# Optimization experiments

Measured on AMD Instinct MI355X. Metric: run time of the kernel, lower is better.

## Reference

```python
import jax, jax.numpy as jnp
import numpy as np

EPS = 1e-10

def _mlp(x, W1, b1, W2, b2):
    # Linear -> ReLU -> Linear (matches _MultiLayerPercep)
    return jnp.maximum(x @ W1 + b1, 0.0) @ W2 + b2

def setup_inputs() -> dict:
    key = jax.random.key(0)
    ks = jax.random.split(key, 24)
    B, P, Q, P2, D = 512, 100, 40, 40, 64
    Nu, Ni, Nr = 100000, 100000, 6

    def lin(k, fi, fo):
        kw, kb = jax.random.split(k)
        s = 1.0 / np.sqrt(fi)
        return (jax.random.uniform(kw, (fi, fo), jnp.float32, -s, s),
                jax.random.uniform(kb, (fo,), jnp.float32, -s, s))

    uids = jax.random.randint(ks[0], (B,), 0, Nu)
    u_item_pad = jnp.stack([jax.random.randint(ks[1], (B, P), 0, Ni),
                            jax.random.randint(ks[2], (B, P), 0, Nr)], axis=-1)
    u_user_pad = jax.random.randint(ks[3], (B, Q), 0, Nu)
    u_user_item_pad = jnp.stack([jax.random.randint(ks[4], (B, Q, P2), 0, Ni),
                                 jax.random.randint(ks[5], (B, Q, P2), 0, Nr)], axis=-1)

    user_table = jax.random.normal(ks[6], (Nu, D), jnp.float32) * 0.1
    item_table = jax.random.normal(ks[7], (Ni, D), jnp.float32) * 0.1
    rate_table = jax.random.normal(ks[8], (Nr, D), jnp.float32) * 0.1

    gv_W1, gv_b1 = lin(ks[9], 2 * D, D)
    gv_W2, gv_b2 = lin(ks[10], D, D)
    atti_W1, atti_b1 = lin(ks[11], 2 * D, D)
    atti_W2, atti_b2 = lin(ks[12], D, 1)
    agg_W, agg_b = lin(ks[13], D, D)
    attu_W1, attu_b1 = lin(ks[14], 2 * D, D)
    attu_W2, attu_b2 = lin(ks[15], D, 1)
    aggn_W, aggn_b = lin(ks[16], D, D)
    cm_W1, cm_b1 = lin(ks[17], 2 * D, D)
    cm_W2, cm_b2 = lin(ks[18], D, D)
    cm_W3, cm_b3 = lin(ks[19], D, D)

    return dict(uids=uids, u_item_pad=u_item_pad, u_user_pad=u_user_pad,
                u_user_item_pad=u_user_item_pad,
                user_table=user_table, item_table=item_table, rate_table=rate_table,
                gv_W1=gv_W1, gv_b1=gv_b1, gv_W2=gv_W2, gv_b2=gv_b2,
                atti_W1=atti_W1, atti_b1=atti_b1, atti_W2=atti_W2, atti_b2=atti_b2,
                agg_W=agg_W, agg_b=agg_b,
                attu_W1=attu_W1, attu_b1=attu_b1, attu_W2=attu_W2, attu_b2=attu_b2,
                aggn_W=aggn_W, aggn_b=aggn_b,
                cm_W1=cm_W1, cm_b1=cm_b1, cm_W2=cm_W2, cm_b2=cm_b2, cm_W3=cm_W3, cm_b3=cm_b3)

def reference(uids, u_item_pad, u_user_pad, u_user_item_pad,
              user_table, item_table, rate_table,
              gv_W1, gv_b1, gv_W2, gv_b2,
              atti_W1, atti_b1, atti_W2, atti_b2,
              agg_W, agg_b,
              attu_W1, attu_b1, attu_W2, attu_b2,
              aggn_W, aggn_b,
              cm_W1, cm_b1, cm_W2, cm_b2, cm_W3, cm_b3):
    f32 = jnp.float32

    # ---- item aggregation branch ----
    q_a = item_table[u_item_pad[:, :, 0]]                      # [B,P,D]
    mask_u = (u_item_pad[:, :, 0] > 0).astype(f32)             # [B,P]
    er = rate_table[u_item_pad[:, :, 1]]                       # [B,P,D]
    x_ia = _mlp(jnp.concatenate([q_a, er], -1), gv_W1, gv_b1, gv_W2, gv_b2)
    p_i = mask_u[..., None] * user_table[uids][:, None, :]     # [B,P,D]
    alpha = _mlp(jnp.concatenate([x_ia, p_i], -1), atti_W1, atti_b1, atti_W2, atti_b2)[..., 0]
    alpha = jnp.exp(alpha) * mask_u
    alpha = alpha / (jnp.sum(alpha, axis=1, keepdims=True) + EPS)
    h_iI = jnp.maximum(jnp.sum(alpha[..., None] * x_ia, axis=1) @ agg_W + agg_b, 0.0)  # [B,D]

    # ---- social branch: per-neighbor item aggregation ----
    q_a_s = item_table[u_user_item_pad[:, :, :, 0]]            # [B,Q,P2,D]
    mask_s = (u_user_item_pad[:, :, :, 0] > 0).astype(f32)     # [B,Q,P2]
    er_s = rate_table[u_user_item_pad[:, :, :, 1]]
    x_ia_s = _mlp(jnp.concatenate([q_a_s, er_s], -1), gv_W1, gv_b1, gv_W2, gv_b2)
    nbr_emb = user_table[u_user_pad]                           # [B,Q,D]
    p_i_s = mask_s[..., None] * nbr_emb[:, :, None, :]
    alpha_s = _mlp(jnp.concatenate([x_ia_s, p_i_s], -1), atti_W1, atti_b1, atti_W2, atti_b2)[..., 0]
    alpha_s = jnp.exp(alpha_s) * mask_s
    alpha_s = alpha_s / (jnp.sum(alpha_s, axis=2, keepdims=True) + EPS)
    h_oI = jnp.maximum(jnp.sum(alpha_s[..., None] * x_ia_s, axis=2) @ agg_W + agg_b, 0.0)  # [B,Q,D]

    # ---- social attention over neighbors ----
    beta = _mlp(jnp.concatenate([h_oI, nbr_emb], -1), attu_W1, attu_b1, attu_W2, attu_b2)[..., 0]
    mask_su = (u_user_pad > 0).astype(f32)
    beta = jnp.exp(beta) * mask_su
    beta = beta / (jnp.sum(beta, axis=1, keepdims=True) + EPS)
    h_iS = jnp.maximum(jnp.sum(beta[..., None] * h_oI, axis=1) @ aggn_W + aggn_b, 0.0)  # [B,D]

    # ---- combine ----
    h = jnp.maximum(jnp.concatenate([h_iI, h_iS], -1) @ cm_W1 + cm_b1, 0.0)
    h = jnp.maximum(h @ cm_W2 + cm_b2, 0.0)
    h = jnp.maximum(h @ cm_W3 + cm_b3, 0.0)
    return h
```

## Files before the change

kernel.cpp:

```cpp
#include <hip/hip_runtime.h>
#include <math.h>

#define EPSV 1e-10f

typedef _Float16 f16x8 __attribute__((ext_vector_type(8)));
typedef _Float16 f16x4 __attribute__((ext_vector_type(4)));
typedef float f32x4 __attribute__((ext_vector_type(4)));

#define OFF_W1T  0
#define OFF_W2T  16384
#define OFF_M2T  24576
#define OFF_X    32768
#define OFF_V    49152
#define SMEM_SZ  54272

__device__ __forceinline__ f16x8 cvt_f16x8(const float4 a, const float4 b) {
  f16x8 h;
  h[0] = (_Float16)a.x; h[1] = (_Float16)a.y; h[2] = (_Float16)a.z; h[3] = (_Float16)a.w;
  h[4] = (_Float16)b.x; h[5] = (_Float16)b.y; h[6] = (_Float16)b.z; h[7] = (_Float16)b.w;
  return h;
}

__global__ __launch_bounds__(256, 2) void agg_kernel(
    const int nSblk,
    const int* __restrict__ idsS, const int* __restrict__ uidS,
    const int* __restrict__ idsI, const int* __restrict__ uidI,
    const float* __restrict__ user_table, const float* __restrict__ item_table,
    const float* __restrict__ rate_table,
    const float* __restrict__ gv_W1, const float* __restrict__ gv_b1,
    const float* __restrict__ gv_W2, const float* __restrict__ gv_b2,
    const float* __restrict__ atti_W1, const float* __restrict__ atti_b1,
    const float* __restrict__ atti_W2, const float* __restrict__ atti_b2,
    const float* __restrict__ agg_W, const float* __restrict__ agg_b,
    float* __restrict__ outS, float* __restrict__ outI) {
  __shared__ __align__(16) char smem[SMEM_SZ];
  const int tid = threadIdx.x;
  const int wave = tid >> 6, lane = tid & 63;
  const int quad = lane >> 4, mrow = lane & 15;

  const bool isS = (int)blockIdx.x < nSblk;
  const int NG = isS ? 16 : 4;
  const int P = isS ? 40 : 100;
  const int nGrp = isS ? 4 : 1;
  const int tpg = isS ? 3 : 8;
  const int* __restrict__ ids = isS ? idsS : idsI;
  const int* __restrict__ uidp = isS ? uidS : uidI;
  float* __restrict__ out = isS ? outS : outI;
  const int gbase = isS ? (int)blockIdx.x * 16 : ((int)blockIdx.x - nSblk) * 4;

  float* sV = (float*)(smem + OFF_V);
  char* smX = smem + OFF_X;
  char* smXw = smX + wave * 4096;
  float* csW = (float*)smXw;

  {
    float* uS = (float*)smX;
    float* AU = (float*)(smem + OFF_W1T);
    for (int t = tid; t < NG * 64; t += 256) {
      const int g = t >> 6, f = t & 63;
      uS[t] = user_table[(size_t)uidp[gbase + g] * 64 + f];
    }
    for (int o = tid; o < 1024; o += 256) {
      const int k = o >> 4, fb = o & 15;
      const float4 v = ((const float4*)(atti_W1 + (64 + k) * 64))[fb];
      const float* vp = (const float*)&v;
#pragma unroll
      for (int c = 0; c < 4; ++c) {
        const int j = fb * 4 + c;
        AU[j * 64 + (((k >> 2) ^ (j & 15)) << 2) + (k & 3)] = vp[c];
      }
    }
  }
  __syncthreads();
  {
    const float4* u4 = (const float4*)smX;
    const float4* a4 = (const float4*)(smem + OFF_W1T);
    for (int t = tid; t < NG * 64; t += 256) {
      const int g = t >> 6, j = t & 63;
      float s = 0.f;
#pragma unroll 4
      for (int kb = 0; kb < 16; ++kb) {
        const float4 uu = u4[g * 16 + kb];
        const float4 aa = a4[j * 16 + (kb ^ (j & 15))];
        s += uu.x * aa.x + uu.y * aa.y + uu.z * aa.z + uu.w * aa.w;
      }
      sV[t] = s;
    }
  }
  __syncthreads();
  {
    for (int o = tid; o < 2048; o += 256) {
      const int k = o >> 4, fb = o & 15;
      const float4 v = ((const float4*)(gv_W1 + k * 64))[fb];
      const float* vp = (const float*)&v;
#pragma unroll
      for (int c = 0; c < 4; ++c) {
        const int n = fb * 4 + c;
        *(_Float16*)(smem + OFF_W1T + n * 256 + ((((k >> 3) ^ (n & 7))) << 4) +
                     ((k & 7) << 1)) = (_Float16)vp[c];
      }
    }
    for (int o = tid; o < 1024; o += 256) {
      const int h = o >> 4, fb = o & 15;
      const float4 v = ((const float4*)(gv_W2 + h * 64))[fb];
      const float* vp = (const float*)&v;
#pragma unroll
      for (int c = 0; c < 4; ++c) {
        const int n = fb * 4 + c;
        *(_Float16*)(smem + OFF_W2T + n * 128 + ((((h >> 3) ^ (n & 7))) << 4) +
                     ((h & 7) << 1)) = (_Float16)vp[c];
      }
    }
    float* sCstP = (float*)smX;
    const int n = tid & 63, jh = tid >> 6;
    float p = 0.f;
#pragma unroll 4
    for (int jj = 0; jj < 16; ++jj) {
      const int j = jh * 16 + jj;
      p = fmaf(gv_b2[j], atti_W1[j * 64 + n], p);
    }
    sCstP[jh * 64 + n] = p;
  }
  float b1r[16], b2v[4], aw2v[4];
#pragma unroll
  for (int nt = 0; nt < 4; ++nt) {
#pragma unroll
    for (int rg = 0; rg < 4; ++rg) b1r[nt * 4 + rg] = gv_b1[nt * 16 + quad * 4 + rg];
    b2v[nt] = gv_b2[nt * 16 + mrow];
    aw2v[nt] = atti_W2[nt * 16 + mrow];
  }
  const float ab2 = atti_b2[0];

  float4 pf[8];
  float pm;
  auto do_prefetch = [&](int gi2, int tt2) {
    const int g2 = gbase + wave + 4 * gi2;
    const int it = tt2 * 16 + mrow;
    int iid = 0, rid = 0;
    float m = 0.f;
    if (it < P) {
      const int2 pr = ((const int2*)ids)[(size_t)g2 * P + it];
      iid = pr.x; rid = pr.y;
      m = pr.x > 0 ? 1.f : 0.f;
    }
    pm = m;
    const float* ib = item_table + (size_t)iid * 64 + quad * 8;
    const float* rb = rate_table + (size_t)rid * 64 + quad * 8;
    pf[0] = ((const float4*)ib)[0];        pf[1] = ((const float4*)ib)[1];
    pf[2] = ((const float4*)(ib + 32))[0]; pf[3] = ((const float4*)(ib + 32))[1];
    pf[4] = ((const float4*)rb)[0];        pf[5] = ((const float4*)rb)[1];
    pf[6] = ((const float4*)(rb + 32))[0]; pf[7] = ((const float4*)(rb + 32))[1];
  };
  do_prefetch(0, 0);
  __syncthreads();
  float cstv[4];
  {
    f16x8 aM[2];
#pragma unroll
    for (int ks = 0; ks < 2; ++ks) {
      f16x8 t;
#pragma unroll
      for (int j = 0; j < 8; ++j)
        t[j] = (_Float16)atti_W1[(ks * 32 + quad * 8 + j) * 64 + (wave * 16 + mrow)];
      aM[ks] = t;
    }
#pragma unroll
    for (int ht = 0; ht < 4; ++ht) {
      f32x4 c = {0.f, 0.f, 0.f, 0.f};
#pragma unroll
      for (int ks = 0; ks < 2; ++ks) {
        const float* s = gv_W2 + (ht * 16 + mrow) * 64 + ks * 32 + quad * 8;
        f16x8 b;
#pragma unroll
        for (int j = 0; j < 8; ++j) b[j] = (_Float16)s[j];
        c = __builtin_amdgcn_mfma_f32_16x16x32_f16(aM[ks], b, c, 0, 0, 0);
      }
      const int h = ht * 16 + mrow;
#pragma unroll
      for (int rg = 0; rg < 4; ++rg) {
        const int n3 = wave * 16 + quad * 4 + rg;
        *(_Float16*)(smem + OFF_M2T + n3 * 128 + ((((h >> 3) ^ (n3 & 7))) << 4) +
                     ((h & 7) << 1)) = (_Float16)c[rg];
      }
    }
    const float* sCstP = (const float*)smX;
#pragma unroll
    for (int nt = 0; nt < 4; ++nt) {
      const int n = nt * 16 + mrow;
      cstv[nt] = atti_b1[n] + sCstP[n] + sCstP[64 + n] + sCstP[128 + n] +
                 sCstP[192 + n];
    }
  }
  __syncthreads();

  f16x8 aW[4][4], bMr[4][2];
#pragma unroll
  for (int nt = 0; nt < 4; ++nt) {
#pragma unroll
    for (int ks = 0; ks < 4; ++ks)
      aW[nt][ks] = *(const f16x8*)(smem + OFF_W1T + (nt * 16 + mrow) * 256 +
                                   (((ks * 4 + quad) ^ (mrow & 7)) << 4));
#pragma unroll
    for (int ks = 0; ks < 2; ++ks)
      bMr[nt][ks] = *(const f16x8*)(smem + OFF_M2T + (nt * 16 + mrow) * 128 +
                                    (((ks * 4 + quad) ^ (mrow & 7)) << 4));
  }

  for (int gi = 0; gi < nGrp; ++gi) {
    const int g = wave + 4 * gi;
    float vv[4];
#pragma unroll
    for (int nt = 0; nt < 4; ++nt) vv[nt] = sV[g * 64 + nt * 16 + mrow];
    float pnum[4] = {0.f, 0.f, 0.f, 0.f};
    float pden = 0.f;
    for (int tt = 0; tt < tpg; ++tt) {
      f16x8 bIn[4];
      bIn[0] = cvt_f16x8(pf[0], pf[1]);
      bIn[1] = cvt_f16x8(pf[2], pf[3]);
      bIn[2] = cvt_f16x8(pf[4], pf[5]);
      bIn[3] = cvt_f16x8(pf[6], pf[7]);
      const float mcur = pm;
      {
        int ngi = gi, ntt = tt + 1;
        if (ntt == tpg) { ntt = 0; ngi = gi + 1; }
        if (ngi < nGrp) do_prefetch(ngi, ntt);
      }
#pragma unroll
      for (int nt = 0; nt < 4; ++nt) {
        f32x4 c = {0.f, 0.f, 0.f, 0.f};
#pragma unroll
        for (int ks = 0; ks < 4; ++ks)
          c = __builtin_amdgcn_mfma_f32_16x16x32_f16(aW[nt][ks], bIn[ks], c, 0, 0, 0);
        f16x4 hv;
#pragma unroll
        for (int rg = 0; rg < 4; ++rg)
          hv[rg] = (_Float16)fmaxf(c[rg] + b1r[nt * 4 + rg], 0.f);
        *(f16x4*)(smXw + mrow * 256 +
                  (((nt * 2 + (quad >> 1)) ^ (mrow & 7)) << 4) +
                  ((quad & 1) << 3)) = hv;
      }
      f16x8 a2[2];
#pragma unroll
      for (int ks = 0; ks < 2; ++ks)
        a2[ks] = *(const f16x8*)(smXw + mrow * 256 +
                                 (((ks * 4 + quad) ^ (mrow & 7)) << 4));
      float mk[4];
#pragma unroll
      for (int rg = 0; rg < 4; ++rg) mk[rg] = __shfl(mcur, quad * 4 + rg);
      f32x4 x2a[4];
      float tl[4] = {0.f, 0.f, 0.f, 0.f};
#pragma unroll
      for (int nt = 0; nt < 4; ++nt) {
        f32x4 c = {0.f, 0.f, 0.f, 0.f}, d = {0.f, 0.f, 0.f, 0.f};
#pragma unroll
        for (int ks = 0; ks < 2; ++ks) {
          const f16x8 bW = *(const f16x8*)(smem + OFF_W2T + (nt * 16 + mrow) * 128 +
                                           (((ks * 4 + quad) ^ (mrow & 7)) << 4));
          c = __builtin_amdgcn_mfma_f32_16x16x32_f16(a2[ks], bW, c, 0, 0, 0);
        }
#pragma unroll
        for (int ks = 0; ks < 2; ++ks)
          d = __builtin_amdgcn_mfma_f32_16x16x32_f16(a2[ks], bMr[nt][ks], d, 0, 0, 0);
#pragma unroll
        for (int rg = 0; rg < 4; ++rg) x2a[nt][rg] = c[rg] + b2v[nt];
#pragma unroll
        for (int rg = 0; rg < 4; ++rg) {
          const float hh = fmaxf(d[rg] + cstv[nt] + mk[rg] * vv[nt], 0.f);
          tl[rg] = fmaf(hh, aw2v[nt], tl[rg]);
        }
      }
      float e[4];
#pragma unroll
      for (int rg = 0; rg < 4; ++rg) {
        float t = tl[rg];
        t += __shfl_xor(t, 1); t += __shfl_xor(t, 2);
        t += __shfl_xor(t, 4); t += __shfl_xor(t, 8);
        e[rg] = __expf(t + ab2) * mk[rg];
        pden += e[rg];
      }
#pragma unroll
      for (int nt = 0; nt < 4; ++nt) {
        pnum[nt] = fmaf(e[0], x2a[nt][0], pnum[nt]);
        pnum[nt] = fmaf(e[1], x2a[nt][1], pnum[nt]);
        pnum[nt] = fmaf(e[2], x2a[nt][2], pnum[nt]);
        pnum[nt] = fmaf(e[3], x2a[nt][3], pnum[nt]);
      }
    }
    float dsum = pden;
    dsum += __shfl_xor(dsum, 16); dsum += __shfl_xor(dsum, 32);
    const float rd = 1.f / (dsum + EPSV);
#pragma unroll
    for (int nt = 0; nt < 4; ++nt) {
      float s = pnum[nt];
      s += __shfl_xor(s, 16); s += __shfl_xor(s, 32);
      if (quad == 0) csW[nt * 16 + mrow] = s * rd;
    }
    float acc = agg_b[lane];
#pragma unroll 8
    for (int k = 0; k < 64; ++k) acc = fmaf(csW[k], agg_W[k * 64 + lane], acc);
    out[(size_t)(gbase + g) * 64 + lane] = fmaxf(acc, 0.f);
  }
}

#define S2_W1T 0
#define S2_X   17408
#define S2_E   26112
#define S2_MSK 26240
#define S2_HB  26368
#define S2_SZ  27904

__global__ __launch_bounds__(128, 2) void stage2_kernel(
    const int* __restrict__ u_user_pad, const float* __restrict__ user_table,
    const float* __restrict__ hoI, const float* __restrict__ hiI,
    const float* __restrict__ attu_W1, const float* __restrict__ attu_b1,
    const float* __restrict__ attu_W2, const float* __restrict__ attu_b2,
    const float* __restrict__ aggn_W, const float* __restrict__ aggn_b,
    const float* __restrict__ cm_W1, const float* __restrict__ cm_b1,
    const float* __restrict__ cm_W2, const float* __restrict__ cm_b2,
    const float* __restrict__ cm_W3, const float* __restrict__ cm_b3,
    float* __restrict__ out) {
  __shared__ __align__(16) char smem[S2_SZ];
  const int tid = threadIdx.x;
  const int wave = tid >> 6, lane = tid & 63;
  const int quad = lane >> 4, mrow = lane & 15;
  const int b = (int)blockIdx.x * 2 + wave;

  char* sW1 = smem + S2_W1T;
  char* sXw = smem + S2_X + wave * 4352;
  float* sE = (float*)(smem + S2_E) + wave * 16;
  float* sM = (float*)(smem + S2_MSK) + wave * 16;
  float* sB = (float*)(smem + S2_HB) + wave * 192;

  for (int o = tid; o < 2048; o += 128) {
    const int k = o >> 4, fb = o & 15;
    const float4 v = ((const float4*)(attu_W1 + k * 64))[fb];
    const float* vp = (const float*)&v;
#pragma unroll
    for (int c = 0; c < 4; ++c) {
      const int n = fb * 4 + c;
      *(_Float16*)(sW1 + n * 272 + ((k >> 3) << 4) + ((k & 7) << 1)) = (_Float16)vp[c];
    }
  }
  float b1v[4], w2v[4];
#pragma unroll
  for (int nt = 0; nt < 4; ++nt) {
    b1v[nt] = attu_b1[nt * 16 + mrow];
    w2v[nt] = attu_W2[nt * 16 + mrow];
  }
  const float b2s = attu_b2[0];

  float4 pa[4], pb[4];
  float msk[4];
  auto pf = [&](int tt) {
#pragma unroll
    for (int k = 0; k < 4; ++k) {
      const int u = lane + (k << 6);
      const int r = u >> 4, bb = u & 15;
      const int q = tt * 16 + r;
      const int qc = q < 40 ? q : 39;
      int uid = 0;
      float m = 0.f;
      if (q < 40) {
        uid = u_user_pad[b * 40 + q];
        m = uid > 0 ? 1.f : 0.f;
      }
      msk[k] = m;
      const float* src = (bb < 8)
                             ? hoI + ((size_t)b * 40 + qc) * 64 + bb * 8
                             : user_table + (size_t)uid * 64 + (bb - 8) * 8;
      pa[k] = ((const float4*)src)[0];
      pb[k] = ((const float4*)src)[1];
    }
  };
  pf(0);
  __syncthreads();

  float numer = 0.f, pden = 0.f;
  for (int tt = 0; tt < 3; ++tt) {
#pragma unroll
    for (int k = 0; k < 4; ++k) {
      const int u = lane + (k << 6);
      const int r = u >> 4, bb = u & 15;
      *(f16x8*)(sXw + r * 272 + (bb << 4)) = cvt_f16x8(pa[k], pb[k]);
      if (bb == 0) sM[r] = msk[k];
    }
    if (tt < 2) pf(tt + 1);
    f16x8 a[4];
#pragma unroll
    for (int ks = 0; ks < 4; ++ks)
      a[ks] = *(const f16x8*)(sXw + mrow * 272 + ((ks * 4 + quad) << 4));
    float mk[4];
#pragma unroll
    for (int rg = 0; rg < 4; ++rg) mk[rg] = sM[quad * 4 + rg];
    float tl[4] = {0.f, 0.f, 0.f, 0.f};
#pragma unroll
    for (int nt = 0; nt < 4; ++nt) {
      f32x4 d = {0.f, 0.f, 0.f, 0.f};
      const int n = nt * 16 + mrow;
#pragma unroll
      for (int ks = 0; ks < 4; ++ks) {
        const f16x8 bW = *(const f16x8*)(sW1 + n * 272 + ((ks * 4 + quad) << 4));
        d = __builtin_amdgcn_mfma_f32_16x16x32_f16(a[ks], bW, d, 0, 0, 0);
      }
#pragma unroll
      for (int rg = 0; rg < 4; ++rg) {
        const float h = fmaxf(d[rg] + b1v[nt], 0.f);
        tl[rg] = fmaf(h, w2v[nt], tl[rg]);
      }
    }
    float e[4];
#pragma unroll
    for (int rg = 0; rg < 4; ++rg) {
      float t = tl[rg];
      t += __shfl_xor(t, 1); t += __shfl_xor(t, 2);
      t += __shfl_xor(t, 4); t += __shfl_xor(t, 8);
      e[rg] = __expf(t + b2s) * mk[rg];
      pden += e[rg];
    }
    if (mrow == 0) {
#pragma unroll
      for (int rg = 0; rg < 4; ++rg) sE[quad * 4 + rg] = e[rg];
    }
#pragma unroll 4
    for (int r = 0; r < 16; ++r) {
      const float er = sE[r];
      const float xv = (float)*(const _Float16*)(sXw + r * 272 + ((lane >> 3) << 4) +
                                                 ((lane & 7) << 1));
      numer = fmaf(er, xv, numer);
    }
  }
  pden += __shfl_xor(pden, 16);
  pden += __shfl_xor(pden, 32);
  const float hagg = numer / (pden + EPSV);

  sB[128 + lane] = hagg;
  sB[lane] = hiI[(size_t)b * 64 + lane];
  float acc = aggn_b[lane];
#pragma unroll 8
  for (int k = 0; k < 64; ++k) acc = fmaf(sB[128 + k], aggn_W[k * 64 + lane], acc);
  sB[64 + lane] = fmaxf(acc, 0.f);
  float c1 = cm_b1[lane];
#pragma unroll 8
  for (int k = 0; k < 128; ++k) c1 = fmaf(sB[k], cm_W1[k * 64 + lane], c1);
  sB[128 + lane] = fmaxf(c1, 0.f);
  float c2 = cm_b2[lane];
#pragma unroll 8
  for (int k = 0; k < 64; ++k) c2 = fmaf(sB[128 + k], cm_W2[k * 64 + lane], c2);
  sB[lane] = fmaxf(c2, 0.f);
  float c3 = cm_b3[lane];
#pragma unroll 8
  for (int k = 0; k < 64; ++k) c3 = fmaf(sB[k], cm_W3[k * 64 + lane], c3);
  out[(size_t)b * 64 + lane] = fmaxf(c3, 0.f);
}

extern "C" void kernel_launch(void* const* d_in, const int* in_sizes, int n_in,
                              void* d_out, int out_size, void* d_ws, size_t ws_size,
                              hipStream_t stream) {
  const int* uids = (const int*)d_in[0];
  const int* u_item_pad = (const int*)d_in[1];
  const int* u_user_pad = (const int*)d_in[2];
  const int* u_user_item_pad = (const int*)d_in[3];
  const float* user_table = (const float*)d_in[4];
  const float* item_table = (const float*)d_in[5];
  const float* rate_table = (const float*)d_in[6];
  const float* gv_W1 = (const float*)d_in[7];
  const float* gv_b1 = (const float*)d_in[8];
  const float* gv_W2 = (const float*)d_in[9];
  const float* gv_b2 = (const float*)d_in[10];
  const float* atti_W1 = (const float*)d_in[11];
  const float* atti_b1 = (const float*)d_in[12];
  const float* atti_W2 = (const float*)d_in[13];
  const float* atti_b2 = (const float*)d_in[14];
  const float* agg_W = (const float*)d_in[15];
  const float* agg_b = (const float*)d_in[16];
  const float* attu_W1 = (const float*)d_in[17];
  const float* attu_b1 = (const float*)d_in[18];
  const float* attu_W2 = (const float*)d_in[19];
  const float* attu_b2 = (const float*)d_in[20];
  const float* aggn_W = (const float*)d_in[21];
  const float* aggn_b = (const float*)d_in[22];
  const float* cm_W1 = (const float*)d_in[23];
  const float* cm_b1 = (const float*)d_in[24];
  const float* cm_W2 = (const float*)d_in[25];
  const float* cm_b2 = (const float*)d_in[26];
  const float* cm_W3 = (const float*)d_in[27];
  const float* cm_b3 = (const float*)d_in[28];
  float* out = (float*)d_out;

  float* hoI = (float*)d_ws;
  float* hiI = hoI + (size_t)512 * 40 * 64;

  agg_kernel<<<1280 + 128, 256, 0, stream>>>(
      1280, u_user_item_pad, u_user_pad, u_item_pad, uids,
      user_table, item_table, rate_table,
      gv_W1, gv_b1, gv_W2, gv_b2,
      atti_W1, atti_b1, atti_W2, atti_b2,
      agg_W, agg_b, hoI, hiI);
  stage2_kernel<<<256, 128, 0, stream>>>(u_user_pad, user_table, hoI, hiI,
                                         attu_W1, attu_b1, attu_W2, attu_b2,
                                         aggn_W, aggn_b,
                                         cm_W1, cm_b1, cm_W2, cm_b2, cm_W3, cm_b3,
                                         out);
}
```

Measured before the change: 290.8 us.

## Pack two groups per MFMA tile with 512-thread blocks to cut padded rows

After: 822.4 us. 2.83x slower.

```diff
diff --git a/kernel.cpp b/kernel.cpp
--- a/kernel.cpp
+++ b/kernel.cpp
@@ -11,8 +11,8 @@
 #define OFF_W2T  16384
 #define OFF_M2T  24576
 #define OFF_X    32768
-#define OFF_V    49152
-#define SMEM_SZ  54272
+#define OFF_V    65536
+#define SMEM_SZ  73728
 
 __device__ __forceinline__ f16x8 cvt_f16x8(const float4 a, const float4 b) {
   f16x8 h;
@@ -21,7 +21,7 @@
   return h;
 }
 
-__global__ __launch_bounds__(256, 2) void agg_kernel(
+__global__ __launch_bounds__(512, 4) void agg_kernel(
     const int nSblk,
     const int* __restrict__ idsS, const int* __restrict__ uidS,
     const int* __restrict__ idsI, const int* __restrict__ uidI,
@@ -39,14 +39,13 @@
   const int quad = lane >> 4, mrow = lane & 15;
 
   const bool isS = (int)blockIdx.x < nSblk;
-  const int NG = isS ? 16 : 4;
+  const int NG = isS ? 32 : 8;
   const int P = isS ? 40 : 100;
-  const int nGrp = isS ? 4 : 1;
-  const int tpg = isS ? 3 : 8;
+  const int rowsplit = isS ? 40 : 112;
   const int* __restrict__ ids = isS ? idsS : idsI;
   const int* __restrict__ uidp = isS ? uidS : uidI;
   float* __restrict__ out = isS ? outS : outI;
-  const int gbase = isS ? (int)blockIdx.x * 16 : ((int)blockIdx.x - nSblk) * 4;
+  const int gbase = isS ? (int)blockIdx.x * 32 : ((int)blockIdx.x - nSblk) * 8;
 
   float* sV = (float*)(smem + OFF_V);
   char* smX = smem + OFF_X;
@@ -56,11 +55,11 @@
   {
     float* uS = (float*)smX;
     float* AU = (float*)(smem + OFF_W1T);
-    for (int t = tid; t < NG * 64; t += 256) {
+    for (int t = tid; t < NG * 64; t += 512) {
       const int g = t >> 6, f = t & 63;
       uS[t] = user_table[(size_t)uidp[gbase + g] * 64 + f];
     }
-    for (int o = tid; o < 1024; o += 256) {
+    for (int o = tid; o < 1024; o += 512) {
       const int k = o >> 4, fb = o & 15;
       const float4 v = ((const float4*)(atti_W1 + (64 + k) * 64))[fb];
       const float* vp = (const float*)&v;
@@ -75,7 +74,7 @@
   {
     const float4* u4 = (const float4*)smX;
     const float4* a4 = (const float4*)(smem + OFF_W1T);
-    for (int t = tid; t < NG * 64; t += 256) {
+    for (int t = tid; t < NG * 64; t += 512) {
       const int g = t >> 6, j = t & 63;
       float s = 0.f;
 #pragma unroll 4
@@ -89,7 +88,7 @@
   }
   __syncthreads();
   {
-    for (int o = tid; o < 2048; o += 256) {
+    for (int o = tid; o < 2048; o += 512) {
       const int k = o >> 4, fb = o & 15;
       const float4 v = ((const float4*)(gv_W1 + k * 64))[fb];
       const float* vp = (const float*)&v;
@@ -100,7 +99,7 @@
                      ((k & 7) << 1)) = (_Float16)vp[c];
       }
     }
-    for (int o = tid; o < 1024; o += 256) {
+    for (int o = tid; o < 1024; o += 512) {
       const int h = o >> 4, fb = o & 15;
       const float4 v = ((const float4*)(gv_W2 + h * 64))[fb];
       const float* vp = (const float*)&v;
@@ -114,9 +113,9 @@
     float* sCstP = (float*)smX;
     const int n = tid & 63, jh = tid >> 6;
     float p = 0.f;
-#pragma unroll 4
-    for (int jj = 0; jj < 16; ++jj) {
-      const int j = jh * 16 + jj;
+#pragma unroll
+    for (int jj = 0; jj < 8; ++jj) {
+      const int j = jh * 8 + jj;
       p = fmaf(gv_b2[j], atti_W1[j * 64 + n], p);
     }
     sCstP[jh * 64 + n] = p;
@@ -133,9 +132,11 @@
 
   float4 pf[8];
   float pm;
-  auto do_prefetch = [&](int gi2, int tt2) {
-    const int g2 = gbase + wave + 4 * gi2;
-    const int it = tt2 * 16 + mrow;
+  auto do_pf = [&](int gA2, int gB2, int tt2) {
+    const int rr = tt2 * 16 + mrow;
+    const bool inB = rr >= rowsplit;
+    const int g2 = inB ? gB2 : gA2;
+    const int it = inB ? rr - rowsplit : rr;
     int iid = 0, rid = 0;
     float m = 0.f;
     if (it < P) {
@@ -151,17 +152,21 @@
     pf[4] = ((const float4*)rb)[0];        pf[5] = ((const float4*)rb)[1];
     pf[6] = ((const float4*)(rb + 32))[0]; pf[7] = ((const float4*)(rb + 32))[1];
   };
-  do_prefetch(0, 0);
+  {
+    const int gA0 = isS ? gbase + wave * 4 : gbase + wave;
+    do_pf(gA0, gA0 + (isS ? 1 : 0), 0);
+  }
   __syncthreads();
   float cstv[4];
   {
+    const int w4 = wave & 3;
     f16x8 aM[2];
 #pragma unroll
     for (int ks = 0; ks < 2; ++ks) {
       f16x8 t;
 #pragma unroll
       for (int j = 0; j < 8; ++j)
-        t[j] = (_Float16)atti_W1[(ks * 32 + quad * 8 + j) * 64 + (wave * 16 + mrow)];
+        t[j] = (_Float16)atti_W1[(ks * 32 + quad * 8 + j) * 64 + (w4 * 16 + mrow)];
       aM[ks] = t;
     }
 #pragma unroll
@@ -178,7 +183,7 @@
       const int h = ht * 16 + mrow;
 #pragma unroll
       for (int rg = 0; rg < 4; ++rg) {
-        const int n3 = wave * 16 + quad * 4 + rg;
+        const int n3 = w4 * 16 + quad * 4 + rg;
         *(_Float16*)(smem + OFF_M2T + n3 * 128 + ((((h >> 3) ^ (n3 & 7))) << 4) +
                      ((h & 7) << 1)) = (_Float16)c[rg];
       }
@@ -187,8 +192,10 @@
 #pragma unroll
     for (int nt = 0; nt < 4; ++nt) {
       const int n = nt * 16 + mrow;
-      cstv[nt] = atti_b1[n] + sCstP[n] + sCstP[64 + n] + sCstP[128 + n] +
-                 sCstP[192 + n];
+      float cs = atti_b1[n];
+#pragma unroll
+      for (int jh = 0; jh < 8; ++jh) cs += sCstP[jh * 64 + n];
+      cstv[nt] = cs;
     }
   }
   __syncthreads();
@@ -206,99 +213,144 @@
                                     (((ks * 4 + quad) ^ (mrow & 7)) << 4));
   }
 
-  for (int gi = 0; gi < nGrp; ++gi) {
-    const int g = wave + 4 * gi;
-    float vv[4];
-#pragma unroll
-    for (int nt = 0; nt < 4; ++nt) vv[nt] = sV[g * 64 + nt * 16 + mrow];
-    float pnum[4] = {0.f, 0.f, 0.f, 0.f};
-    float pden = 0.f;
-    for (int tt = 0; tt < tpg; ++tt) {
-      f16x8 bIn[4];
-      bIn[0] = cvt_f16x8(pf[0], pf[1]);
-      bIn[1] = cvt_f16x8(pf[2], pf[3]);
-      bIn[2] = cvt_f16x8(pf[4], pf[5]);
-      bIn[3] = cvt_f16x8(pf[6], pf[7]);
-      const float mcur = pm;
-      {
-        int ngi = gi, ntt = tt + 1;
-        if (ntt == tpg) { ntt = 0; ngi = gi + 1; }
-        if (ngi < nGrp) do_prefetch(ngi, ntt);
-      }
-#pragma unroll
-      for (int nt = 0; nt < 4; ++nt) {
-        f32x4 c = {0.f, 0.f, 0.f, 0.f};
-#pragma unroll
-        for (int ks = 0; ks < 4; ++ks)
-          c = __builtin_amdgcn_mfma_f32_16x16x32_f16(aW[nt][ks], bIn[ks], c, 0, 0, 0);
-        f16x4 hv;
-#pragma unroll
-        for (int rg = 0; rg < 4; ++rg)
-          hv[rg] = (_Float16)fmaxf(c[rg] + b1r[nt * 4 + rg], 0.f);
-        *(f16x4*)(smXw + mrow * 256 +
-                  (((nt * 2 + (quad >> 1)) ^ (mrow & 7)) << 4) +
-                  ((quad & 1) << 3)) = hv;
-      }
-      f16x8 a2[2];
+  float vvA[4], vvB[4];
+  float pnA[4], pnB[4], pdA, pdB;
+
+  auto tile = [&](int mode, int gAn, int gBn, int ttn, bool dopf) {
+    f16x8 bIn[4];
+    bIn[0] = cvt_f16x8(pf[0], pf[1]);
+    bIn[1] = cvt_f16x8(pf[2], pf[3]);
+    bIn[2] = cvt_f16x8(pf[4], pf[5]);
+    bIn[3] = cvt_f16x8(pf[6], pf[7]);
+    const float mcur = pm;
+    if (dopf) do_pf(gAn, gBn, ttn);
+#pragma unroll
+    for (int nt = 0; nt < 4; ++nt) {
+      f32x4 c = {0.f, 0.f, 0.f, 0.f};
+#pragma unroll
+      for (int ks = 0; ks < 4; ++ks)
+        c = __builtin_amdgcn_mfma_f32_16x16x32_f16(aW[nt][ks], bIn[ks], c, 0, 0, 0);
+      f16x4 hv;
+#pragma unroll
+      for (int rg = 0; rg < 4; ++rg)
+        hv[rg] = (_Float16)fmaxf(c[rg] + b1r[nt * 4 + rg], 0.f);
+      *(f16x4*)(smXw + mrow * 256 +
+                (((nt * 2 + (quad >> 1)) ^ (mrow & 7)) << 4) +
+                ((quad & 1) << 3)) = hv;
+    }
+    f16x8 a2[2];
+#pragma unroll
+    for (int ks = 0; ks < 2; ++ks)
+      a2[ks] = *(const f16x8*)(smXw + mrow * 256 +
+                               (((ks * 4 + quad) ^ (mrow & 7)) << 4));
+    float mk[4];
+#pragma unroll
+    for (int rg = 0; rg < 4; ++rg) mk[rg] = __shfl(mcur, quad * 4 + rg);
+    float vcur[4];
+#pragma unroll
+    for (int nt = 0; nt < 4; ++nt)
+      vcur[nt] = (mode == 0) ? vvA[nt]
+               : (mode == 2) ? vvB[nt]
+                             : (quad < 2 ? vvA[nt] : vvB[nt]);
+    f32x4 x2a[4];
+    float tl[4] = {0.f, 0.f, 0.f, 0.f};
+#pragma unroll
+    for (int nt = 0; nt < 4; ++nt) {
+      f32x4 c = {0.f, 0.f, 0.f, 0.f}, d = {0.f, 0.f, 0.f, 0.f};
+#pragma unroll
+      for (int ks = 0; ks < 2; ++ks) {
+        const f16x8 bW = *(const f16x8*)(smem + OFF_W2T + (nt * 16 + mrow) * 128 +
+                                         (((ks * 4 + quad) ^ (mrow & 7)) << 4));
+        c = __builtin_amdgcn_mfma_f32_16x16x32_f16(a2[ks], bW, c, 0, 0, 0);
+      }
 #pragma unroll
       for (int ks = 0; ks < 2; ++ks)
-        a2[ks] = *(const f16x8*)(smXw + mrow * 256 +
-                                 (((ks * 4 + quad) ^ (mrow & 7)) << 4));
-      float mk[4];
-#pragma unroll
-      for (int rg = 0; rg < 4; ++rg) mk[rg] = __shfl(mcur, quad * 4 + rg);
-      f32x4 x2a[4];
-      float tl[4] = {0.f, 0.f, 0.f, 0.f};
-#pragma unroll
-      for (int nt = 0; nt < 4; ++nt) {
-        f32x4 c = {0.f, 0.f, 0.f, 0.f}, d = {0.f, 0.f, 0.f, 0.f};
-#pragma unroll
-        for (int ks = 0; ks < 2; ++ks) {
-          const f16x8 bW = *(const f16x8*)(smem + OFF_W2T + (nt * 16 + mrow) * 128 +
-                                           (((ks * 4 + quad) ^ (mrow & 7)) << 4));
-          c = __builtin_amdgcn_mfma_f32_16x16x32_f16(a2[ks], bW, c, 0, 0, 0);
-        }
-#pragma unroll
-        for (int ks = 0; ks < 2; ++ks)
-          d = __builtin_amdgcn_mfma_f32_16x16x32_f16(a2[ks], bMr[nt][ks], d, 0, 0, 0);
-#pragma unroll
-        for (int rg = 0; rg < 4; ++rg) x2a[nt][rg] = c[rg] + b2v[nt];
-#pragma unroll
-        for (int rg = 0; rg < 4; ++rg) {
-          const float hh = fmaxf(d[rg] + cstv[nt] + mk[rg] * vv[nt], 0.f);
-          tl[rg] = fmaf(hh, aw2v[nt], tl[rg]);
-        }
-      }
-      float e[4];
+        d = __builtin_amdgcn_mfma_f32_16x16x32_f16(a2[ks], bMr[nt][ks], d, 0, 0, 0);
+#pragma unroll
+      for (int rg = 0; rg < 4; ++rg) x2a[nt][rg] = c[rg] + b2v[nt];
 #pragma unroll
       for (int rg = 0; rg < 4; ++rg) {
-        float t = tl[rg];
-        t += __shfl_xor(t, 1); t += __shfl_xor(t, 2);
-        t += __shfl_xor(t, 4); t += __shfl_xor(t, 8);
-        e[rg] = __expf(t + ab2) * mk[rg];
-        pden += e[rg];
-      }
-#pragma unroll
-      for (int nt = 0; nt < 4; ++nt) {
-        pnum[nt] = fmaf(e[0], x2a[nt][0], pnum[nt]);
-        pnum[nt] = fmaf(e[1], x2a[nt][1], pnum[nt]);
-        pnum[nt] = fmaf(e[2], x2a[nt][2], pnum[nt]);
-        pnum[nt] = fmaf(e[3], x2a[nt][3], pnum[nt]);
-      }
-    }
-    float dsum = pden;
+        const float hh = fmaxf(d[rg] + cstv[nt] + mk[rg] * vcur[nt], 0.f);
+        tl[rg] = fmaf(hh, aw2v[nt], tl[rg]);
+      }
+    }
+    float eA[4], eB[4];
+#pragma unroll
+    for (int rg = 0; rg < 4; ++rg) {
+      float t = tl[rg];
+      t += __shfl_xor(t, 1); t += __shfl_xor(t, 2);
+      t += __shfl_xor(t, 4); t += __shfl_xor(t, 8);
+      const float ee = __expf(t + ab2) * mk[rg];
+      eA[rg] = (mode == 0) ? ee : (mode == 2) ? 0.f : (quad < 2 ? ee : 0.f);
+      eB[rg] = (mode == 2) ? ee : (mode == 0) ? 0.f : (quad < 2 ? 0.f : ee);
+      pdA += eA[rg];
+      pdB += eB[rg];
+    }
+#pragma unroll
+    for (int nt = 0; nt < 4; ++nt) {
+      if (mode != 2) {
+        pnA[nt] = fmaf(eA[0], x2a[nt][0], pnA[nt]);
+        pnA[nt] = fmaf(eA[1], x2a[nt][1], pnA[nt]);
+        pnA[nt] = fmaf(eA[2], x2a[nt][2], pnA[nt]);
+        pnA[nt] = fmaf(eA[3], x2a[nt][3], pnA[nt]);
+      }
+      if (mode != 0) {
+        pnB[nt] = fmaf(eB[0], x2a[nt][0], pnB[nt]);
+        pnB[nt] = fmaf(eB[1], x2a[nt][1], pnB[nt]);
+        pnB[nt] = fmaf(eB[2], x2a[nt][2], pnB[nt]);
+        pnB[nt] = fmaf(eB[3], x2a[nt][3], pnB[nt]);
+      }
+    }
+  };
+
+  auto flush = [&](int gg, float* pn, float pd) {
+    float dsum = pd;
     dsum += __shfl_xor(dsum, 16); dsum += __shfl_xor(dsum, 32);
     const float rd = 1.f / (dsum + EPSV);
 #pragma unroll
     for (int nt = 0; nt < 4; ++nt) {
-      float s = pnum[nt];
+      float s = pn[nt];
       s += __shfl_xor(s, 16); s += __shfl_xor(s, 32);
       if (quad == 0) csW[nt * 16 + mrow] = s * rd;
     }
     float acc = agg_b[lane];
 #pragma unroll 8
     for (int k = 0; k < 64; ++k) acc = fmaf(csW[k], agg_W[k * 64 + lane], acc);
-    out[(size_t)(gbase + g) * 64 + lane] = fmaxf(acc, 0.f);
+    out[(size_t)gg * 64 + lane] = fmaxf(acc, 0.f);
+  };
+
+  if (isS) {
+#pragma unroll
+    for (int pi = 0; pi < 2; ++pi) {
+      const int gA = gbase + wave * 4 + 2 * pi, gB = gA + 1;
+      const int gl = wave * 4 + 2 * pi;
+#pragma unroll
+      for (int nt = 0; nt < 4; ++nt) {
+        vvA[nt] = sV[gl * 64 + nt * 16 + mrow];
+        vvB[nt] = sV[(gl + 1) * 64 + nt * 16 + mrow];
+        pnA[nt] = 0.f; pnB[nt] = 0.f;
+      }
+      pdA = 0.f; pdB = 0.f;
+      tile(0, gA, gB, 1, true);
+      tile(0, gA, gB, 2, true);
+      tile(1, gA, gB, 3, true);
+      tile(2, gA, gB, 4, true);
+      tile(2, gA + 2, gB + 2, 0, pi == 0);
+      flush(gA, pnA, pdA);
+      flush(gB, pnB, pdB);
+    }
+  } else {
+    const int gA = gbase + wave;
+#pragma unroll
+    for (int nt = 0; nt < 4; ++nt) {
+      vvA[nt] = sV[wave * 64 + nt * 16 + mrow];
+      vvB[nt] = 0.f;
+      pnA[nt] = 0.f; pnB[nt] = 0.f;
+    }
+    pdA = 0.f; pdB = 0.f;
+#pragma unroll
+    for (int tt = 0; tt < 7; ++tt) tile(0, gA, gA, tt + 1, tt < 6);
+    flush(gA, pnA, pdA);
   }
 }
 
@@ -351,7 +403,7 @@
 
   float4 pa[4], pb[4];
   float msk[4];
-  auto pf = [&](int tt) {
+  auto pfn = [&](int tt) {
 #pragma unroll
     for (int k = 0; k < 4; ++k) {
       const int u = lane + (k << 6);
@@ -372,7 +424,7 @@
       pb[k] = ((const float4*)src)[1];
     }
   };
-  pf(0);
+  pfn(0);
   __syncthreads();
 
   float numer = 0.f, pden = 0.f;
@@ -384,7 +436,7 @@
       *(f16x8*)(sXw + r * 272 + (bb << 4)) = cvt_f16x8(pa[k], pb[k]);
       if (bb == 0) sM[r] = msk[k];
     }
-    if (tt < 2) pf(tt + 1);
+    if (tt < 2) pfn(tt + 1);
     f16x8 a[4];
 #pragma unroll
     for (int ks = 0; ks < 4; ++ks)
@@ -490,8 +542,8 @@
   float* hoI = (float*)d_ws;
   float* hiI = hoI + (size_t)512 * 40 * 64;
 
-  agg_kernel<<<1280 + 128, 256, 0, stream>>>(
-      1280, u_user_item_pad, u_user_pad, u_item_pad, uids,
+  agg_kernel<<<640 + 64, 512, 0, stream>>>(
+      640, u_user_item_pad, u_user_pad, u_item_pad, uids,
       user_table, item_table, rate_table,
       gv_W1, gv_b1, gv_W2, gv_b2,
       atti_W1, atti_b1, atti_W2, atti_b2,
```
